# Kernel optimization log

Measured on AMD Instinct MI355X. Metric: run time of the kernel, lower is better.

Reference implementation:

```python
import jax, jax.numpy as jnp
import numpy as np

B, S, D, H, DQ, DV = 4, 1024, 1024, 16, 64, 64
EPS = 1e-5  # torch LayerNorm default


def setup_inputs() -> dict:
    key = jax.random.key(0)
    ks = jax.random.split(key, 6)
    x = jax.random.normal(ks[0], (B, S, D), dtype=jnp.float32)
    scale = 0.02
    return {
        "query_sequences": x,
        "key_sequences": x,   # self-attention: identical tensors
        "value_sequences": x,
        "key_value_sequence_lengths": jax.random.randint(ks[1], (B,), 512, S + 1, dtype=jnp.int32),
        "ln_gamma": jnp.ones((D,), jnp.float32),
        "ln_beta": jnp.zeros((D,), jnp.float32),
        "Wq": scale * jax.random.normal(ks[2], (D, H * DQ), jnp.float32),
        "bq": jnp.zeros((H * DQ,), jnp.float32),
        "Wk": scale * jax.random.normal(ks[3], (D, H * DQ), jnp.float32),
        "bk": jnp.zeros((H * DQ,), jnp.float32),
        "Wv": scale * jax.random.normal(ks[4], (D, H * DV), jnp.float32),
        "bv": jnp.zeros((H * DV,), jnp.float32),
    }


def _layer_norm(x, gamma, beta):
    mu = jnp.mean(x, axis=-1, keepdims=True)
    var = jnp.mean(jnp.square(x - mu), axis=-1, keepdims=True)
    return (x - mu) * jax.lax.rsqrt(var + EPS) * gamma + beta


def reference(query_sequences, key_sequences, value_sequences,
              key_value_sequence_lengths, ln_gamma, ln_beta,
              Wq, bq, Wk, bk, Wv, bv):
    # self-attention path (query/key/value sequences are identical):
    # pre-LayerNorm applied to all three, causal + pad masking, dropout=0.
    x_in = query_sequences
    xn = _layer_norm(x_in, ln_gamma, ln_beta)

    q = (xn @ Wq + bq).reshape(B, S, H, DQ).transpose(0, 2, 1, 3)  # (B,H,S,DQ)
    k = (xn @ Wk + bk).reshape(B, S, H, DQ).transpose(0, 2, 1, 3)
    v = (xn @ Wv + bv).reshape(B, S, H, DV).transpose(0, 2, 1, 3)

    scores = jnp.einsum("bhqd,bhkd->bhqk", q, k) * (1.0 / np.sqrt(DQ))

    kv_pos = jnp.arange(S)
    pad_mask = kv_pos[None, None, None, :] < key_value_sequence_lengths[:, None, None, None]
    causal = jnp.tril(jnp.ones((S, S), dtype=bool))[None, None]
    mask = pad_mask & causal
    scores = jnp.where(mask, scores, -jnp.inf)

    attn = jax.nn.softmax(scores, axis=-1)  # (B,H,S,S)

    out = jnp.einsum("bhqk,bhkd->bhqd", attn, v)          # (B,H,S,DV)
    out = out.transpose(0, 2, 1, 3).reshape(B, S, H * DV)  # (B,S,D)
    # d_model == n_heads*d_values -> cast_output is Identity; residual is plain sum
    seq = x_in + out
    return seq, attn
```

## Files before the change

### kernel.cpp

```cpp
#include <hip/hip_runtime.h>
#include <stdint.h>

#define BB 4
#define SS 1024
#define DD 1024
#define HH 16

typedef __attribute__((ext_vector_type(8))) __bf16 bf16x8;
typedef __attribute__((ext_vector_type(4))) __bf16 bf16x4;
typedef __attribute__((ext_vector_type(4))) float f32x4;

__device__ __forceinline__ unsigned short f2bf(float f) {
  union { float ff; uint32_t u; } a; a.ff = f;
  uint32_t r = a.u + 0x7fffu + ((a.u >> 16) & 1u);
  return (unsigned short)(r >> 16);
}

__device__ __forceinline__ float bf2f(unsigned short u) {
  union { uint32_t uu; float ff; } a; a.uu = ((uint32_t)u) << 16;
  return a.ff;
}

__device__ __forceinline__ f32x4 mfma16(bf16x8 a, bf16x8 b, f32x4 c) {
  return __builtin_amdgcn_mfma_f32_16x16x32_bf16(a, b, c, 0, 0, 0);
}

__device__ __forceinline__ uint32_t cvtpk(float a, float b) {
  uint32_t r;
  asm("v_cvt_pk_bf16_f32 %0, %1, %2" : "=v"(r) : "v"(a), "v"(b));
  return r;
}

__device__ __forceinline__ void async16(const unsigned short* g, unsigned short* l) {
  __builtin_amdgcn_global_load_lds(
      (__attribute__((address_space(1))) void*)(g),
      (__attribute__((address_space(3))) void*)(l), 16u, 0, 0u);
}

__device__ __forceinline__ void nt_store4(float* p, f32x4 v) {
  __builtin_nontemporal_store(v, (f32x4*)p);
}

__global__ __launch_bounds__(256) void wtrans_kernel(const float* __restrict__ Wq,
                                                     const float* __restrict__ Wk,
                                                     const float* __restrict__ Wv,
                                                     unsigned short* __restrict__ Wtq,
                                                     unsigned short* __restrict__ Wtk,
                                                     unsigned short* __restrict__ Wtv) {
  __shared__ unsigned short t[64][65];
  const int z = blockIdx.z;
  const float* W = (z == 0) ? Wq : (z == 1) ? Wk : Wv;
  unsigned short* Wt = (z == 0) ? Wtq : (z == 1) ? Wtk : Wtv;
  const int k0 = blockIdx.x * 64, n0 = blockIdx.y * 64;
  const int c = threadIdx.x & 63, r0 = threadIdx.x >> 6;
#pragma unroll
  for (int i = 0; i < 16; ++i) {
    int r = i * 4 + r0;
    t[r][c] = f2bf(W[(size_t)(k0 + r) * DD + n0 + c]);
  }
  __syncthreads();
#pragma unroll
  for (int i = 0; i < 16; ++i) {
    int n = i * 4 + r0;
    Wt[(size_t)(n0 + n) * DD + k0 + c] = t[c][n];
  }
}

__global__ __launch_bounds__(256) void ln_kernel(const float* __restrict__ X,
                                                 const float* __restrict__ gamma,
                                                 const float* __restrict__ beta,
                                                 unsigned short* __restrict__ Xn) {
  const int row = blockIdx.x;
  const int tid = threadIdx.x;
  const float* xr = X + (size_t)row * DD;
  float4 v = ((const float4*)xr)[tid];
  float s = v.x + v.y + v.z + v.w;
  float s2 = v.x * v.x + v.y * v.y + v.z * v.z + v.w * v.w;
#pragma unroll
  for (int off = 1; off < 64; off <<= 1) {
    s += __shfl_xor(s, off);
    s2 += __shfl_xor(s2, off);
  }
  __shared__ float red[8];
  const int wv = tid >> 6, lane = tid & 63;
  if (lane == 0) { red[wv] = s; red[4 + wv] = s2; }
  __syncthreads();
  s = red[0] + red[1] + red[2] + red[3];
  s2 = red[4] + red[5] + red[6] + red[7];
  const float mu = s * (1.0f / DD);
  const float rs = rsqrtf(s2 * (1.0f / DD) - mu * mu + 1e-5f);
  float4 g = ((const float4*)gamma)[tid];
  float4 bt = ((const float4*)beta)[tid];
  ushort4 o;
  o.x = f2bf((v.x - mu) * rs * g.x + bt.x);
  o.y = f2bf((v.y - mu) * rs * g.y + bt.y);
  o.z = f2bf((v.z - mu) * rs * g.z + bt.z);
  o.w = f2bf((v.w - mu) * rs * g.w + bt.w);
  ((ushort4*)(Xn + (size_t)row * DD))[tid] = o;
}

__global__ __launch_bounds__(256) void gemm_qkv_kernel(
    const unsigned short* __restrict__ Xn,
    const unsigned short* __restrict__ Wtq, const unsigned short* __restrict__ Wtk,
    const unsigned short* __restrict__ Wtv,
    const float* __restrict__ bq, const float* __restrict__ bk, const float* __restrict__ bv,
    unsigned short* __restrict__ Qb, unsigned short* __restrict__ Kb,
    unsigned short* __restrict__ Vt) {
  __shared__ __align__(16) unsigned short smem[128 * 136];
  unsigned short* sA = smem;
  unsigned short* sB = smem + 128 * 32;
  const int z = blockIdx.z;
  const unsigned short* Wt = (z == 0) ? Wtq : (z == 1) ? Wtk : Wtv;
  const float* bias = (z == 0) ? bq : (z == 1) ? bk : bv;
  const int tid = threadIdx.x;
  const int lane = tid & 63, wv = tid >> 6;
  const int quad = lane >> 4, l16 = lane & 15;
  const int m0 = blockIdx.x * 128, n0 = blockIdx.y * 128;
  const int wm = (wv & 1) * 64, wn = (wv >> 1) * 64;

  f32x4 acc[4][4];
#pragma unroll
  for (int i = 0; i < 4; ++i)
#pragma unroll
    for (int j = 0; j < 4; ++j) acc[i][j] = (f32x4){0.f, 0.f, 0.f, 0.f};

  for (int kt = 0; kt < DD; kt += 32) {
    __syncthreads();
#pragma unroll
    for (int it = 0; it < 2; ++it) {
      const int c = it * 256 + tid;
      const int row = c >> 2, kc = c & 3;
      async16(Xn + (size_t)(m0 + row) * DD + kt + kc * 8, &sA[(it * 256 + wv * 64) * 8]);
      async16(Wt + (size_t)(n0 + row) * DD + kt + kc * 8, &sB[(it * 256 + wv * 64) * 8]);
    }
    __syncthreads();
    bf16x8 af[4], bfr[4];
#pragma unroll
    for (int i = 0; i < 4; ++i) af[i] = *(const bf16x8*)&sA[(wm + i * 16 + l16) * 32 + quad * 8];
#pragma unroll
    for (int j = 0; j < 4; ++j) bfr[j] = *(const bf16x8*)&sB[(wn + j * 16 + l16) * 32 + quad * 8];
#pragma unroll
    for (int i = 0; i < 4; ++i)
#pragma unroll
      for (int j = 0; j < 4; ++j) acc[i][j] = mfma16(af[i], bfr[j], acc[i][j]);
  }

  __syncthreads();
  if (z < 2) {
    unsigned short* sC = smem;
#pragma unroll
    for (int i = 0; i < 4; ++i) {
      const int lr0 = wm + i * 16 + quad * 4;
#pragma unroll
      for (int j = 0; j < 4; ++j) {
        const int lc = wn + j * 16 + l16;
        const float bb = bias[n0 + lc];
#pragma unroll
        for (int r = 0; r < 4; ++r) sC[(lr0 + r) * 136 + lc] = f2bf(acc[i][j][r] + bb);
      }
    }
    __syncthreads();
    unsigned short* Out = (z == 0) ? Qb : Kb;
    const int rr = tid >> 4, c8 = (tid & 15) * 8;
#pragma unroll
    for (int it = 0; it < 8; ++it) {
      const int row = it * 16 + rr;
      *(uint4*)&Out[(size_t)(m0 + row) * DD + n0 + c8] = *(const uint4*)&sC[row * 136 + c8];
    }
  } else {
    unsigned short* sC = smem;
#pragma unroll
    for (int i = 0; i < 4; ++i) {
      const int lr0 = wm + i * 16 + quad * 4;
#pragma unroll
      for (int j = 0; j < 4; ++j) {
        const int lc = wn + j * 16 + l16;
        const float bb = bias[n0 + lc];
#pragma unroll
        for (int r = 0; r < 4; ++r) sC[lc * 136 + lr0 + r] = f2bf(acc[i][j][r] + bb);
      }
    }
    __syncthreads();
    const int b = m0 >> 10, s0 = m0 & 1023;
    const int rr = tid >> 4, c8 = (tid & 15) * 8;
#pragma unroll
    for (int it = 0; it < 8; ++it) {
      const int row = it * 16 + rr;
      const int n = n0 + row;
      unsigned short* dst =
          &Vt[((size_t)((b * HH + (n >> 6)) * 64 + (n & 63))) * SS + s0 + c8];
      *(uint4*)dst = *(const uint4*)&sC[row * 136 + c8];
    }
  }
}

__global__ __launch_bounds__(256) void attn_kernel(
    const unsigned short* __restrict__ Qb, const unsigned short* __restrict__ Kb,
    const unsigned short* __restrict__ Vt, const float* __restrict__ X,
    const int* __restrict__ lens, float* __restrict__ seq_out,
    float* __restrict__ attn_out) {
  __shared__ __align__(16) unsigned short smem[2 * 128 * 64];
  unsigned short* sQV = smem;
  unsigned short* sK = smem + 128 * 64;

  const int tid = threadIdx.x;
  const int lane = tid & 63, wv = tid >> 6;
  const int quad = lane >> 4, l16 = lane & 15;
  const int h = blockIdx.y, b = blockIdx.z;
  const int qt = (b & 2) ? (7 - (int)blockIdx.x) : (int)blockIdx.x;
  const int q0 = qt * 128;
  const int len = lens[b];
  const int KE = min(q0 + 128, len);
  const int NKT = (KE + 127) >> 7;
  const float SCL = 0.1803368801111204f;
  const int s7 = l16 & 7;

#pragma unroll
  for (int it = 0; it < 4; ++it) {
    const int c = it * 256 + tid;
    const int row = c >> 3, ch = (c & 7) ^ (row & 7);
    async16(Qb + (size_t)(b * SS + q0 + row) * DD + h * 64 + ch * 8,
            &sQV[(it * 256 + wv * 64) * 8]);
  }
  __syncthreads();

  bf16x8 qf[2][2];
#pragma unroll
  for (int i = 0; i < 2; ++i)
#pragma unroll
    for (int dd = 0; dd < 2; ++dd)
      qf[i][dd] = *(const bf16x8*)
          &sQV[(wv * 32 + i * 16 + l16) * 64 + ((dd * 4 + quad) ^ s7) * 8];

  float lsum[2] = {0.f, 0.f};

  for (int kt = 0; kt < NKT; ++kt) {
    const int k0 = kt * 128;
    __syncthreads();
#pragma unroll
    for (int it = 0; it < 4; ++it) {
      const int c = it * 256 + tid;
      const int row = c >> 3, ch = (c & 7) ^ (row & 7);
      async16(Kb + (size_t)(b * SS + k0 + row) * DD + h * 64 + ch * 8,
              &sK[(it * 256 + wv * 64) * 8]);
    }
    __syncthreads();
    const bool edge = (kt == qt) || (k0 + 128 > len);
#pragma unroll
    for (int j = 0; j < 8; ++j) {
      const bf16x8 kf0 = *(const bf16x8*)&sK[(j * 16 + l16) * 64 + ((0 + quad) ^ s7) * 8];
      const bf16x8 kf1 = *(const bf16x8*)&sK[(j * 16 + l16) * 64 + ((4 + quad) ^ s7) * 8];
      const int kb = k0 + j * 16 + quad * 4;
#pragma unroll
      for (int i = 0; i < 2; ++i) {
        f32x4 sc = (f32x4){0.f, 0.f, 0.f, 0.f};
        sc = mfma16(kf0, qf[i][0], sc);
        sc = mfma16(kf1, qf[i][1], sc);
        const int qq = q0 + wv * 32 + i * 16 + l16;
#pragma unroll
        for (int r = 0; r < 4; ++r) {
          float sv = sc[r] * SCL;
          if (edge && ((kb + r > qq) || (kb + r >= len))) sv = -1e30f;
          lsum[i] += __builtin_amdgcn_exp2f(sv);
        }
      }
    }
  }

  float linv[2];
#pragma unroll
  for (int i = 0; i < 2; ++i) {
    float l = lsum[i];
    l += __shfl_xor(l, 16);
    l += __shfl_xor(l, 32);
    linv[i] = 1.0f / l;
  }

  f32x4 oacc[2][4];
#pragma unroll
  for (int i = 0; i < 2; ++i)
#pragma unroll
    for (int jv = 0; jv < 4; ++jv) oacc[i][jv] = (f32x4){0.f, 0.f, 0.f, 0.f};

  const size_t abase = (size_t)(b * HH + h) * SS * SS;
  float* const arowA = attn_out + abase + (size_t)(q0 + wv * 32 + l16) * SS;
  float* const arowB = arowA + (size_t)16 * SS;

  for (int kt = 0; kt < NKT; ++kt) {
    const int k0 = kt * 128;
    __syncthreads();
#pragma unroll
    for (int it = 0; it < 4; ++it) {
      const int c = it * 256 + tid;
      const int krow = c >> 3, kch = (c & 7) ^ (krow & 7);
      async16(Kb + (size_t)(b * SS + k0 + krow) * DD + h * 64 + kch * 8,
              &sK[(it * 256 + wv * 64) * 8]);
      const int vrow = c >> 4, vch = (c & 15) ^ (vrow & 15);
      async16(Vt + ((size_t)((b * HH + h) * 64 + vrow)) * SS + k0 + vch * 8,
              &sQV[(it * 256 + wv * 64) * 8]);
    }
    __syncthreads();
    const bool edge = (kt == qt) || (k0 + 128 > len);

    uint32_t afw[2][4][4];
#pragma unroll
    for (int j = 0; j < 8; ++j) {
      const bf16x8 kf0 = *(const bf16x8*)&sK[(j * 16 + l16) * 64 + ((0 + quad) ^ s7) * 8];
      const bf16x8 kf1 = *(const bf16x8*)&sK[(j * 16 + l16) * 64 + ((4 + quad) ^ s7) * 8];
      const int kb = k0 + j * 16 + quad * 4;
#pragma unroll
      for (int i = 0; i < 2; ++i) {
        f32x4 sc = (f32x4){0.f, 0.f, 0.f, 0.f};
        sc = mfma16(kf0, qf[i][0], sc);
        sc = mfma16(kf1, qf[i][1], sc);
        const int qq = q0 + wv * 32 + i * 16 + l16;
        f32x4 p;
#pragma unroll
        for (int r = 0; r < 4; ++r) {
          float sv = sc[r] * SCL;
          if (edge && ((kb + r > qq) || (kb + r >= len))) sv = -1e30f;
          p[r] = __builtin_amdgcn_exp2f(sv) * linv[i];
        }
        nt_store4((i == 0 ? arowA : arowB) + kb, p);
        afw[i][j >> 1][(j & 1) * 2 + 0] = cvtpk(p[0], p[1]);
        afw[i][j >> 1][(j & 1) * 2 + 1] = cvtpk(p[2], p[3]);
      }
    }

#pragma unroll
    for (int kk = 0; kk < 4; ++kk) {
      union { bf16x8 v8; bf16x4 v4[2]; } vfu[4];
      const int g1 = kk * 4 + (quad >> 1);
      const int boff = (quad & 1) * 8;
#pragma unroll
      for (int jv = 0; jv < 4; ++jv) {
        const char* rowp = (const char*)(sQV + (jv * 16 + l16) * 128);
        vfu[jv].v4[0] = *(const bf16x4*)(rowp + ((g1 ^ l16) * 16 + boff));
        vfu[jv].v4[1] = *(const bf16x4*)(rowp + (((g1 + 2) ^ l16) * 16 + boff));
      }
#pragma unroll
      for (int i = 0; i < 2; ++i) {
        union { uint32_t w[4]; bf16x8 v8; } pu;
        pu.w[0] = afw[i][kk][0];
        pu.w[1] = afw[i][kk][1];
        pu.w[2] = afw[i][kk][2];
        pu.w[3] = afw[i][kk][3];
#pragma unroll
        for (int jv = 0; jv < 4; ++jv) oacc[i][jv] = mfma16(pu.v8, vfu[jv].v8, oacc[i][jv]);
      }
    }
  }

  const int Z = SS - NKT * 128;
  if (Z > 0) {
    const int rr0 = tid >> 3;
    const int cf = (tid & 7) * 4;
    const f32x4 zz = (f32x4){0.f, 0.f, 0.f, 0.f};
    for (int rr = rr0; rr < 128; rr += 32) {
      float* dst = attn_out + abase + (size_t)(q0 + rr) * SS + NKT * 128 + cf;
      for (int c8 = 0; c8 < (Z >> 5); ++c8) nt_store4(dst + c8 * 32, zz);
    }
  }

  __syncthreads();
  {
    float* sPf = (float*)smem + wv * 2048;
#pragma unroll
    for (int i = 0; i < 2; ++i)
#pragma unroll
      for (int jv = 0; jv < 4; ++jv)
#pragma unroll
        for (int r = 0; r < 4; ++r)
          sPf[(i * 16 + quad * 4 + r) * 64 + jv * 16 + l16] = oacc[i][jv][r];
    const int rr = lane >> 4, c4 = (lane & 15) * 4;
#pragma unroll
    for (int it = 0; it < 8; ++it) {
      const int lrow = it * 4 + rr;
      const size_t idx = (size_t)(b * SS + q0 + wv * 32 + lrow) * DD + h * 64 + c4;
      float4 o = *(const float4*)&sPf[lrow * 64 + c4];
      float4 x = *(const float4*)&X[idx];
      o.x += x.x; o.y += x.y; o.z += x.z; o.w += x.w;
      *(float4*)&seq_out[idx] = o;
    }
  }
}

extern "C" void kernel_launch(void* const* d_in, const int* in_sizes, int n_in,
                              void* d_out, int out_size, void* d_ws, size_t ws_size,
                              hipStream_t stream) {
  (void)in_sizes; (void)n_in; (void)out_size; (void)ws_size;
  const float* X     = (const float*)d_in[0];
  const int*   lens  = (const int*)d_in[3];
  const float* gamma = (const float*)d_in[4];
  const float* beta  = (const float*)d_in[5];
  const float* Wq    = (const float*)d_in[6];
  const float* bq    = (const float*)d_in[7];
  const float* Wk    = (const float*)d_in[8];
  const float* bk    = (const float*)d_in[9];
  const float* Wv    = (const float*)d_in[10];
  const float* bv    = (const float*)d_in[11];

  char* ws = (char*)d_ws;
  unsigned short* Xn  = (unsigned short*)(ws);
  unsigned short* Qb  = (unsigned short*)(ws + ((size_t)8  << 20));
  unsigned short* Kb  = (unsigned short*)(ws + ((size_t)16 << 20));
  unsigned short* Vt  = (unsigned short*)(ws + ((size_t)24 << 20));
  unsigned short* Wtq = (unsigned short*)(ws + ((size_t)32 << 20));
  unsigned short* Wtk = (unsigned short*)(ws + ((size_t)34 << 20));
  unsigned short* Wtv = (unsigned short*)(ws + ((size_t)36 << 20));

  float* seq_out  = (float*)d_out;
  float* attn_out = seq_out + (size_t)BB * SS * DD;

  wtrans_kernel<<<dim3(16, 16, 3), 256, 0, stream>>>(Wq, Wk, Wv, Wtq, Wtk, Wtv);
  ln_kernel<<<dim3(BB * SS), 256, 0, stream>>>(X, gamma, beta, Xn);
  gemm_qkv_kernel<<<dim3(32, 8, 3), 256, 0, stream>>>(Xn, Wtq, Wtk, Wtv, bq, bk, bv, Qb, Kb, Vt);
  attn_kernel<<<dim3(8, HH, BB), 256, 0, stream>>>(Qb, Kb, Vt, X, lens, seq_out, attn_out);
}
```

Before: 419.9 us.

## Double-buffer LDS tiles in QKV GEMM and attention with async prefetch

Both the QKV projection GEMM and the attention kernel now use two LDS buffers per operand. The next K/V (or A/B) tile is issued with async loads before computing on the current one, so one barrier per iteration replaces two. The attention kernel also prefetches the first K/V tiles for the second pass during the last iteration of the row-sum pass, and wraps the MFMA sequences in s_setprio to favour matrix issue. The cost is doubled LDS in the attention kernel (64KB instead of 32KB), which may lower occupancy.

```diff
diff --git a/kernel.cpp b/kernel.cpp
--- a/kernel.cpp
+++ b/kernel.cpp
@@ -107,8 +107,10 @@
     unsigned short* __restrict__ Qb, unsigned short* __restrict__ Kb,
     unsigned short* __restrict__ Vt) {
   __shared__ __align__(16) unsigned short smem[128 * 136];
-  unsigned short* sA = smem;
-  unsigned short* sB = smem + 128 * 32;
+  unsigned short* const sA0 = smem;
+  unsigned short* const sB0 = smem + 4096;
+  unsigned short* const sA1 = smem + 8192;
+  unsigned short* const sB1 = smem + 12288;
   const int z = blockIdx.z;
   const unsigned short* Wt = (z == 0) ? Wtq : (z == 1) ? Wtk : Wtv;
   const float* bias = (z == 0) ? bq : (z == 1) ? bk : bv;
@@ -124,8 +126,7 @@
 #pragma unroll
     for (int j = 0; j < 4; ++j) acc[i][j] = (f32x4){0.f, 0.f, 0.f, 0.f};
 
-  for (int kt = 0; kt < DD; kt += 32) {
-    __syncthreads();
+  auto stage = [&](int kt, unsigned short* sA, unsigned short* sB) {
 #pragma unroll
     for (int it = 0; it < 2; ++it) {
       const int c = it * 256 + tid;
@@ -133,19 +134,28 @@
       async16(Xn + (size_t)(m0 + row) * DD + kt + kc * 8, &sA[(it * 256 + wv * 64) * 8]);
       async16(Wt + (size_t)(n0 + row) * DD + kt + kc * 8, &sB[(it * 256 + wv * 64) * 8]);
     }
+  };
+
+  stage(0, sA0, sB0);
+  __syncthreads();
+
+  for (int kt = 0; kt < DD; kt += 32) {
+    const int par = (kt >> 5) & 1;
+    unsigned short* const sA = par ? sA1 : sA0;
+    unsigned short* const sB = par ? sB1 : sB0;
+    if (kt + 32 < DD) stage(kt + 32, par ? sA0 : sA1, par ? sB0 : sB1);
+    bf16x8 af[4], bfr[4];
+#pragma unroll
+    for (int i = 0; i < 4; ++i) af[i] = *(const bf16x8*)&sA[(wm + i * 16 + l16) * 32 + quad * 8];
+#pragma unroll
+    for (int j = 0; j < 4; ++j) bfr[j] = *(const bf16x8*)&sB[(wn + j * 16 + l16) * 32 + quad * 8];
+#pragma unroll
+    for (int i = 0; i < 4; ++i)
+#pragma unroll
+      for (int j = 0; j < 4; ++j) acc[i][j] = mfma16(af[i], bfr[j], acc[i][j]);
     __syncthreads();
-    bf16x8 af[4], bfr[4];
-#pragma unroll
-    for (int i = 0; i < 4; ++i) af[i] = *(const bf16x8*)&sA[(wm + i * 16 + l16) * 32 + quad * 8];
-#pragma unroll
-    for (int j = 0; j < 4; ++j) bfr[j] = *(const bf16x8*)&sB[(wn + j * 16 + l16) * 32 + quad * 8];
-#pragma unroll
-    for (int i = 0; i < 4; ++i)
-#pragma unroll
-      for (int j = 0; j < 4; ++j) acc[i][j] = mfma16(af[i], bfr[j], acc[i][j]);
-  }
-
-  __syncthreads();
+  }
+
   if (z < 2) {
     unsigned short* sC = smem;
 #pragma unroll
@@ -199,9 +209,11 @@
     const unsigned short* __restrict__ Vt, const float* __restrict__ X,
     const int* __restrict__ lens, float* __restrict__ seq_out,
     float* __restrict__ attn_out) {
-  __shared__ __align__(16) unsigned short smem[2 * 128 * 64];
-  unsigned short* sQV = smem;
-  unsigned short* sK = smem + 128 * 64;
+  __shared__ __align__(16) unsigned short smem[4 * 128 * 64];
+  unsigned short* const sK0 = smem;
+  unsigned short* const sK1 = smem + 8192;
+  unsigned short* const sV0 = smem + 16384;
+  unsigned short* const sV1 = smem + 24576;
 
   const int tid = threadIdx.x;
   const int lane = tid & 63, wv = tid >> 6;
@@ -215,13 +227,33 @@
   const float SCL = 0.1803368801111204f;
   const int s7 = l16 & 7;
 
+  auto stageK = [&](int k0, unsigned short* dst) {
+#pragma unroll
+    for (int it = 0; it < 4; ++it) {
+      const int c = it * 256 + tid;
+      const int row = c >> 3, ch = (c & 7) ^ (row & 7);
+      async16(Kb + (size_t)(b * SS + k0 + row) * DD + h * 64 + ch * 8,
+              &dst[(it * 256 + wv * 64) * 8]);
+    }
+  };
+  auto stageV = [&](int k0, unsigned short* dst) {
+#pragma unroll
+    for (int it = 0; it < 4; ++it) {
+      const int c = it * 256 + tid;
+      const int row = c >> 4, ch = (c & 15) ^ (row & 15);
+      async16(Vt + ((size_t)((b * HH + h) * 64 + row)) * SS + k0 + ch * 8,
+              &dst[(it * 256 + wv * 64) * 8]);
+    }
+  };
+
 #pragma unroll
   for (int it = 0; it < 4; ++it) {
     const int c = it * 256 + tid;
     const int row = c >> 3, ch = (c & 7) ^ (row & 7);
     async16(Qb + (size_t)(b * SS + q0 + row) * DD + h * 64 + ch * 8,
-            &sQV[(it * 256 + wv * 64) * 8]);
-  }
+            &sV0[(it * 256 + wv * 64) * 8]);
+  }
+  stageK(0, sK0);
   __syncthreads();
 
   bf16x8 qf[2][2];
@@ -230,32 +262,34 @@
 #pragma unroll
     for (int dd = 0; dd < 2; ++dd)
       qf[i][dd] = *(const bf16x8*)
-          &sQV[(wv * 32 + i * 16 + l16) * 64 + ((dd * 4 + quad) ^ s7) * 8];
+          &sV0[(wv * 32 + i * 16 + l16) * 64 + ((dd * 4 + quad) ^ s7) * 8];
 
   float lsum[2] = {0.f, 0.f};
+  int par = 0;
 
   for (int kt = 0; kt < NKT; ++kt) {
     const int k0 = kt * 128;
-    __syncthreads();
-#pragma unroll
-    for (int it = 0; it < 4; ++it) {
-      const int c = it * 256 + tid;
-      const int row = c >> 3, ch = (c & 7) ^ (row & 7);
-      async16(Kb + (size_t)(b * SS + k0 + row) * DD + h * 64 + ch * 8,
-              &sK[(it * 256 + wv * 64) * 8]);
-    }
-    __syncthreads();
+    const int nxt = par ^ 1;
+    unsigned short* const Kcur = par ? sK1 : sK0;
+    if (kt + 1 < NKT) {
+      stageK((kt + 1) * 128, nxt ? sK1 : sK0);
+    } else {
+      stageK(0, nxt ? sK1 : sK0);
+      stageV(0, nxt ? sV1 : sV0);
+    }
     const bool edge = (kt == qt) || (k0 + 128 > len);
 #pragma unroll
     for (int j = 0; j < 8; ++j) {
-      const bf16x8 kf0 = *(const bf16x8*)&sK[(j * 16 + l16) * 64 + ((0 + quad) ^ s7) * 8];
-      const bf16x8 kf1 = *(const bf16x8*)&sK[(j * 16 + l16) * 64 + ((4 + quad) ^ s7) * 8];
+      const bf16x8 kf0 = *(const bf16x8*)&Kcur[(j * 16 + l16) * 64 + ((0 + quad) ^ s7) * 8];
+      const bf16x8 kf1 = *(const bf16x8*)&Kcur[(j * 16 + l16) * 64 + ((4 + quad) ^ s7) * 8];
       const int kb = k0 + j * 16 + quad * 4;
 #pragma unroll
       for (int i = 0; i < 2; ++i) {
         f32x4 sc = (f32x4){0.f, 0.f, 0.f, 0.f};
+        __builtin_amdgcn_s_setprio(1);
         sc = mfma16(kf0, qf[i][0], sc);
         sc = mfma16(kf1, qf[i][1], sc);
+        __builtin_amdgcn_s_setprio(0);
         const int qq = q0 + wv * 32 + i * 16 + l16;
 #pragma unroll
         for (int r = 0; r < 4; ++r) {
@@ -265,6 +299,8 @@
         }
       }
     }
+    __syncthreads();
+    par = nxt;
   }
 
   float linv[2];
@@ -288,31 +324,28 @@
 
   for (int kt = 0; kt < NKT; ++kt) {
     const int k0 = kt * 128;
-    __syncthreads();
-#pragma unroll
-    for (int it = 0; it < 4; ++it) {
-      const int c = it * 256 + tid;
-      const int krow = c >> 3, kch = (c & 7) ^ (krow & 7);
-      async16(Kb + (size_t)(b * SS + k0 + krow) * DD + h * 64 + kch * 8,
-              &sK[(it * 256 + wv * 64) * 8]);
-      const int vrow = c >> 4, vch = (c & 15) ^ (vrow & 15);
-      async16(Vt + ((size_t)((b * HH + h) * 64 + vrow)) * SS + k0 + vch * 8,
-              &sQV[(it * 256 + wv * 64) * 8]);
-    }
-    __syncthreads();
+    const int nxt = par ^ 1;
+    unsigned short* const Kcur = par ? sK1 : sK0;
+    unsigned short* const Vcur = par ? sV1 : sV0;
+    if (kt + 1 < NKT) {
+      stageK((kt + 1) * 128, nxt ? sK1 : sK0);
+      stageV((kt + 1) * 128, nxt ? sV1 : sV0);
+    }
     const bool edge = (kt == qt) || (k0 + 128 > len);
 
     uint32_t afw[2][4][4];
 #pragma unroll
     for (int j = 0; j < 8; ++j) {
-      const bf16x8 kf0 = *(const bf16x8*)&sK[(j * 16 + l16) * 64 + ((0 + quad) ^ s7) * 8];
-      const bf16x8 kf1 = *(const bf16x8*)&sK[(j * 16 + l16) * 64 + ((4 + quad) ^ s7) * 8];
+      const bf16x8 kf0 = *(const bf16x8*)&Kcur[(j * 16 + l16) * 64 + ((0 + quad) ^ s7) * 8];
+      const bf16x8 kf1 = *(const bf16x8*)&Kcur[(j * 16 + l16) * 64 + ((4 + quad) ^ s7) * 8];
       const int kb = k0 + j * 16 + quad * 4;
 #pragma unroll
       for (int i = 0; i < 2; ++i) {
         f32x4 sc = (f32x4){0.f, 0.f, 0.f, 0.f};
+        __builtin_amdgcn_s_setprio(1);
         sc = mfma16(kf0, qf[i][0], sc);
         sc = mfma16(kf1, qf[i][1], sc);
+        __builtin_amdgcn_s_setprio(0);
         const int qq = q0 + wv * 32 + i * 16 + l16;
         f32x4 p;
 #pragma unroll
@@ -334,10 +367,11 @@
       const int boff = (quad & 1) * 8;
 #pragma unroll
       for (int jv = 0; jv < 4; ++jv) {
-        const char* rowp = (const char*)(sQV + (jv * 16 + l16) * 128);
+        const char* rowp = (const char*)(Vcur + (jv * 16 + l16) * 128);
         vfu[jv].v4[0] = *(const bf16x4*)(rowp + ((g1 ^ l16) * 16 + boff));
         vfu[jv].v4[1] = *(const bf16x4*)(rowp + (((g1 + 2) ^ l16) * 16 + boff));
       }
+      __builtin_amdgcn_s_setprio(1);
 #pragma unroll
       for (int i = 0; i < 2; ++i) {
         union { uint32_t w[4]; bf16x8 v8; } pu;
@@ -348,7 +382,10 @@
 #pragma unroll
         for (int jv = 0; jv < 4; ++jv) oacc[i][jv] = mfma16(pu.v8, vfu[jv].v8, oacc[i][jv]);
       }
-    }
+      __builtin_amdgcn_s_setprio(0);
+    }
+    __syncthreads();
+    par = nxt;
   }
 
   const int Z = SS - NKT * 128;
```

After: 422.4 us. About the same (+0.6%).
